# Performance work log

Measured on AMD Instinct MI355X. Metric: run time of the kernel, lower is better.

Reference implementation:

```python
import jax, jax.numpy as jnp
import numpy as np

N_NODES = 100000
N_EDGES = 1600000
IN_FEATS = 128
NUM_HEADS = 4
OUT_FEATS = 32
NUM_ETYPES = 8
DROP_BLOCKS = 4


def setup_inputs() -> dict:
    key = jax.random.key(0)
    k1, k2, k3, k4, k5 = jax.random.split(key, 5)
    feat = jax.random.normal(k1, (N_NODES, IN_FEATS), dtype=jnp.float32)
    e_feat = jax.random.randint(k2, (N_EDGES,), 0, NUM_ETYPES, dtype=jnp.int32)
    src = jax.random.randint(k3, (N_EDGES,), 0, N_NODES, dtype=jnp.int32)
    dst = jax.random.randint(k4, (N_EDGES,), 0, N_NODES, dtype=jnp.int32)
    kf, ke = jax.random.split(k5)
    # xavier_normal with relu gain for fc: std = gain * sqrt(2/(fan_in+fan_out))
    gain = float(np.sqrt(2.0))
    std = gain * float(np.sqrt(2.0 / (IN_FEATS + NUM_HEADS * OUT_FEATS)))
    fc_weight = jax.random.normal(kf, (NUM_HEADS * OUT_FEATS, IN_FEATS), dtype=jnp.float32) * std
    # edge_emb initialized with normal_()
    edge_emb = jax.random.normal(ke, (NUM_ETYPES, NUM_HEADS), dtype=jnp.float32)
    return {"feat": feat, "fc_weight": fc_weight, "edge_emb": edge_emb,
            "e_feat": e_feat, "src": src, "dst": dst, "drop_blocks": DROP_BLOCKS}


def _edge_softmax(e, dst, n_nodes):
    # segmented softmax over incoming edges per destination node, per head
    # e: (E, H)
    m = jax.ops.segment_max(e, dst, num_segments=n_nodes)      # (N, H)
    z = jnp.exp(e - m[dst])                                    # (E, H)
    s = jax.ops.segment_sum(z, dst, num_segments=n_nodes)      # (N, H)
    return z / s[dst]


def reference(feat, fc_weight, edge_emb, e_feat, src, dst, drop_blocks):
    n = feat.shape[0]
    H = edge_emb.shape[1]
    D = fc_weight.shape[0] // H
    # fc projection -> (N, H, D); feat_drop is identity (p=0 / eval)
    ft = (feat @ fc_weight.T).reshape(n, H, D)
    # edge type embedding logits (E, H)
    ee = edge_emb[e_feat]
    attn = _edge_softmax(ee, dst, n)                           # (E, H)
    # mcdropedge with attn_drop p=0: attn broadcast over blocks is identity scaling
    # u_mul_e + sum: gather src features, scale by attn, scatter-sum into dst
    msg = ft[src] * attn[:, :, None]                           # (E, H, D)
    rst = jax.ops.segment_sum(msg, dst, num_segments=n)        # (N, H, D)
    # attn returned with mcdropedge expansion shape (E, H, drop_blocks, 1)
    attn_out = jnp.broadcast_to(attn[:, :, None], (attn.shape[0], H, drop_blocks))[..., None]
    return rst, attn_out
```

## Files before the change

kernel.cpp:

```cpp
#include <hip/hip_runtime.h>


typedef short short8 __attribute__((ext_vector_type(8)));
typedef unsigned short ushort8 __attribute__((ext_vector_type(8)));
typedef float f32x4 __attribute__((ext_vector_type(4)));

__device__ inline unsigned short f2bf(float x) {
    unsigned u = __builtin_bit_cast(unsigned, x);
    u += 0x7FFFu + ((u >> 16) & 1u);
    return (unsigned short)(u >> 16);
}

__device__ inline short8 cvt8(float4 lo, float4 hi) {
    short8 t;
    t[0] = (short)f2bf(lo.x); t[1] = (short)f2bf(lo.y);
    t[2] = (short)f2bf(lo.z); t[3] = (short)f2bf(lo.w);
    t[4] = (short)f2bf(hi.x); t[5] = (short)f2bf(hi.y);
    t[6] = (short)f2bf(hi.z); t[7] = (short)f2bf(hi.w);
    return t;
}

__device__ inline void nt_store4(float* p, float a, float b, float c, float d) {
    f32x4 v = (f32x4){a, b, c, d};
    __builtin_nontemporal_store(v, (f32x4*)p);
}

__global__ __launch_bounds__(256) void k_bcnt(const int* __restrict__ dst,
                                              unsigned* __restrict__ gpart, int E,
                                              const float* __restrict__ W,
                                              unsigned short* __restrict__ Wb) {
    __shared__ unsigned l[256];
    int tid = threadIdx.x;
    if (blockIdx.x < 8) {
        int i = blockIdx.x * 2048 + tid * 8;
        float4 lo = *(const float4*)(W + i);
        float4 hi = *(const float4*)(W + i + 4);
        *(ushort8*)(Wb + i) = __builtin_bit_cast(ushort8, cvt8(lo, hi));
    }
    l[tid] = 0;
    __syncthreads();
    int base = blockIdx.x * 4096;
#pragma unroll
    for (int j = 0; j < 16; ++j) {
        int e = base + j * 256 + tid;
        if (e < E) atomicAdd(&l[(unsigned)dst[e] >> 9], 1u);
    }
    __syncthreads();
    gpart[blockIdx.x * 256 + tid] = l[tid];
}

__global__ __launch_bounds__(256) void k_bscan(const unsigned* __restrict__ gpart,
                                               int nchunk,
                                               unsigned* __restrict__ gbase,
                                               unsigned* __restrict__ gcur) {
    __shared__ unsigned s[256];
    int t = threadIdx.x;
    unsigned sum = 0;
    int r = 0;
    for (; r + 4 <= nchunk; r += 4) {
        unsigned a0 = gpart[(r + 0) * 256 + t];
        unsigned a1 = gpart[(r + 1) * 256 + t];
        unsigned a2 = gpart[(r + 2) * 256 + t];
        unsigned a3 = gpart[(r + 3) * 256 + t];
        sum += a0 + a1 + a2 + a3;
    }
    for (; r < nchunk; ++r) sum += gpart[r * 256 + t];
    unsigned orig = sum;
    s[t] = sum;
    __syncthreads();
    for (int of = 1; of < 256; of <<= 1) {
        unsigned v = (t >= of) ? s[t - of] : 0u;
        __syncthreads();
        s[t] += v;
        __syncthreads();
    }
    unsigned eb = s[t] - orig;
    gbase[t] = eb;
    gcur[t] = eb;
}

__global__ __launch_bounds__(256) void k_partgemm(
        const int* __restrict__ src, const int* __restrict__ dst,
        const int* __restrict__ ef, unsigned* __restrict__ gcur,
        unsigned* __restrict__ csr2, int E, int nbuk, int partBlocks,
        const float* __restrict__ feat, const unsigned short* __restrict__ Wb,
        unsigned short* __restrict__ ftb, int N) {
    __shared__ unsigned short Sb[128 * 136];
    int tid = threadIdx.x;

    if (blockIdx.x < (unsigned)partBlocks) {
        unsigned* lcnt = (unsigned*)Sb;
        unsigned* lbase = lcnt + 256;
        unsigned* lcur = lbase + 256;
        unsigned* gw2 = lcur + 256;
        unsigned* stp = gw2 + 256;
        unsigned short* stb = (unsigned short*)(stp + 4096);
        int bid = blockIdx.x;
        lcnt[tid] = 0;
        __syncthreads();

        int cb = bid * 4096;
        int cc = E - cb; if (cc > 4096) cc = 4096;

        unsigned pay[16];
        unsigned short bk[16];
#pragma unroll
        for (int j = 0; j < 16; ++j) {
            int idx = j * 256 + tid;
            if (idx < cc) {
                int e = cb + idx;
                unsigned d = (unsigned)dst[e];
                pay[j] = (unsigned)src[e] | ((unsigned)ef[e] << 17) | ((d & 511u) << 20);
                bk[j] = (unsigned short)(d >> 9);
                atomicAdd(&lcnt[bk[j]], 1u);
            }
        }
        __syncthreads();
        lbase[tid] = lcnt[tid];
        __syncthreads();
        for (int of = 1; of < 256; of <<= 1) {
            unsigned v = (tid >= of) ? lbase[tid - of] : 0u;
            __syncthreads();
            lbase[tid] += v;
            __syncthreads();
        }
        unsigned eb = lbase[tid] - lcnt[tid];
        __syncthreads();
        lbase[tid] = eb;
        lcur[tid] = eb;
        __syncthreads();
#pragma unroll
        for (int j = 0; j < 16; ++j) {
            int idx = j * 256 + tid;
            if (idx < cc) {
                unsigned lpos = atomicAdd(&lcur[bk[j]], 1u);
                stp[lpos] = pay[j];
                stb[lpos] = bk[j];
            }
        }
        if (tid < nbuk && lcnt[tid]) gw2[tid] = atomicAdd(&gcur[tid], lcnt[tid]);
        __syncthreads();
#pragma unroll
        for (int j = 0; j < 16; ++j) {
            int i = j * 256 + tid;
            if (i < cc) {
                unsigned b = stb[i];
                csr2[gw2[b] + (i - lbase[b])] = stp[i];
            }
        }
        return;
    }

    int row0 = (blockIdx.x - partBlocks) * 128;

#pragma unroll
    for (int it = 0; it < 8; ++it) {
        int idx = it * 2048 + tid * 8;
        int r = idx >> 7, c = idx & 127;
        ushort8 v = *(const ushort8*)(Wb + idx);
        *(ushort8*)((char*)Sb + (((unsigned)(r * 256 + c * 2)) ^ (unsigned)((r & 7) << 4))) = v;
    }
    __syncthreads();

    int wv = tid >> 6, lane = tid & 63;
    int rl = lane & 15;
    unsigned swz = (unsigned)((lane & 7) << 4);
    int kq = (lane >> 4) * 16;
    int ko = (lane >> 4) * 8;

    int ra0 = row0 + wv * 32 + rl;
    int ra1 = ra0 + 16;
    int rc0 = ra0 < N - 1 ? ra0 : N - 1;
    int rc1 = ra1 < N - 1 ? ra1 : N - 1;
    const float* ap0 = feat + (size_t)rc0 * 128 + ko;
    const float* ap1 = feat + (size_t)rc1 * 128 + ko;

    f32x4 acc[2][8];
#pragma unroll
    for (int rt = 0; rt < 2; ++rt)
#pragma unroll
        for (int jt = 0; jt < 8; ++jt)
            acc[rt][jt] = (f32x4){0.f, 0.f, 0.f, 0.f};

    const char* Bb = (const char*)Sb;

    float4 l0 = *(const float4*)(ap0);
    float4 h0 = *(const float4*)(ap0 + 4);
    float4 l1 = *(const float4*)(ap1);
    float4 h1 = *(const float4*)(ap1 + 4);

#pragma unroll 1
    for (int kk = 0; kk < 4; ++kk) {
        short8 a0 = cvt8(l0, h0);
        short8 a1 = cvt8(l1, h1);
        int kn = kk < 3 ? kk + 1 : 3;
        l0 = *(const float4*)(ap0 + kn * 32);
        h0 = *(const float4*)(ap0 + kn * 32 + 4);
        l1 = *(const float4*)(ap1 + kn * 32);
        h1 = *(const float4*)(ap1 + kn * 32 + 4);
        int kb = kk * 64 + kq;
#pragma unroll
        for (int jt = 0; jt < 8; ++jt) {
            short8 bj = *(const short8*)(Bb + (((unsigned)((jt * 16 + rl) * 256 + kb)) ^ swz));
            acc[0][jt] = __builtin_amdgcn_mfma_f32_16x16x32_bf16(a0, bj, acc[0][jt], 0, 0, 0);
            acc[1][jt] = __builtin_amdgcn_mfma_f32_16x16x32_bf16(a1, bj, acc[1][jt], 0, 0, 0);
        }
    }

    __syncthreads();
#pragma unroll
    for (int rt = 0; rt < 2; ++rt) {
        int rbase = wv * 32 + rt * 16 + ((lane >> 4) << 2);
#pragma unroll
        for (int jt = 0; jt < 8; ++jt) {
            int col = jt * 16 + rl;
#pragma unroll
            for (int rg = 0; rg < 4; ++rg)
                Sb[(rbase + rg) * 136 + col] = f2bf(acc[rt][jt][rg]);
        }
    }
    __syncthreads();
#pragma unroll
    for (int g = 0; g < 8; ++g) {
        int rloc = g * 16 + (tid >> 4);
        int cc = (tid & 15) * 8;
        int gr = row0 + rloc;
        if (gr < N) {
            ushort8 v = *(const ushort8*)(&Sb[rloc * 136 + cc]);
            *(ushort8*)(ftb + (size_t)gr * 128 + cc) = v;
        }
    }
}

__global__ __launch_bounds__(256) void k_bsort2(const unsigned* __restrict__ csr2,
                                                const unsigned* __restrict__ gbase,
                                                const unsigned* __restrict__ gend,
                                                const float* __restrict__ emb,
                                                unsigned* __restrict__ csr,
                                                unsigned* __restrict__ offs,
                                                unsigned* __restrict__ deg,
                                                float* __restrict__ stats, int N) {
    __shared__ unsigned cnt8[512 * 8];
    __shared__ unsigned degL[512];
    __shared__ unsigned offsL[512];
    __shared__ unsigned curL[512];
    __shared__ unsigned tmp[256];
    __shared__ float se[32];
    int b = blockIdx.x, tid = threadIdx.x;
    if (tid < 32) se[tid] = emb[tid];
#pragma unroll
    for (int i = 0; i < 16; ++i) cnt8[i * 256 + tid] = 0u;
    __syncthreads();
    unsigned r0 = gbase[b], r1 = gend[b];
    for (unsigned i = r0 + tid; i < r1; i += 256) {
        unsigned en = csr2[i];
        atomicAdd(&cnt8[((en >> 20) & 511u) * 8u + ((en >> 17) & 7u)], 1u);
    }
    __syncthreads();
    int n0 = tid * 2, n1 = tid * 2 + 1;
    unsigned d0 = 0, d1 = 0;
#pragma unroll
    for (int k = 0; k < 8; ++k) { d0 += cnt8[n0 * 8 + k]; d1 += cnt8[n1 * 8 + k]; }
    degL[n0] = d0; degL[n1] = d1;
    tmp[tid] = d0 + d1;
    __syncthreads();
    for (int of = 1; of < 256; of <<= 1) {
        unsigned v = (tid >= of) ? tmp[tid - of] : 0u;
        __syncthreads();
        tmp[tid] += v;
        __syncthreads();
    }
    unsigned eb = tmp[tid] - (d0 + d1);
    offsL[n0] = eb;        curL[n0] = eb;
    offsL[n1] = eb + d0;   curL[n1] = eb + d0;
#pragma unroll
    for (int q = 0; q < 2; ++q) {
        int nl = tid * 2 + q;
        int gn = b * 512 + nl;
        if (gn < N) {
            offs[gn] = r0 + offsL[nl];
            unsigned dg = degL[nl];
            deg[gn] = dg;
            const unsigned* c = &cnt8[nl * 8];
#pragma unroll
            for (int h = 0; h < 4; ++h) {
                float m = -3.4e38f;
#pragma unroll
                for (int tt = 0; tt < 8; ++tt)
                    if (c[tt]) m = fmaxf(m, se[tt * 4 + h]);
                float s = 0.f;
#pragma unroll
                for (int tt = 0; tt < 8; ++tt)
                    if (c[tt]) s += (float)c[tt] * expf(se[tt * 4 + h] - m);
                stats[(size_t)gn * 8 + h] = m;
                stats[(size_t)gn * 8 + 4 + h] = dg ? (1.0f / s) : 0.0f;
            }
        }
    }
    __syncthreads();
    for (unsigned i = r0 + tid; i < r1; i += 256) {
        unsigned en = csr2[i];
        unsigned nlo = (en >> 20) & 511u;
        unsigned tt = (en >> 17) & 7u;
        unsigned pos = r0 + atomicAdd(&curL[nlo], 1u);
        csr[pos] = (en & 0x1FFFFu) | (tt << 20);
    }
}

__global__ __launch_bounds__(256) void k_aggattn(
        const unsigned* __restrict__ csr, const unsigned* __restrict__ offs,
        const unsigned* __restrict__ deg, const float* __restrict__ stats,
        const float* __restrict__ emb, const uint4* __restrict__ ft4,
        float* __restrict__ rst, int N, int aggBlocks,
        const int* __restrict__ e_feat, const int* __restrict__ dst,
        float* __restrict__ ao, int E) {
    __shared__ float sbuf[4 * 257];
    int tid = threadIdx.x;

    if (blockIdx.x >= (unsigned)aggBlocks) {
        int bid = blockIdx.x - aggBlocks;
        int e = bid * 256 + tid;
        float a0 = 0.f, a1 = 0.f, a2 = 0.f, a3 = 0.f;
        if (e < E) {
            int tt = e_feat[e];
            int d = dst[e];
            const float4* st4 = (const float4*)(stats + (size_t)d * 8);
            float4 m4 = st4[0], i4 = st4[1];
            float4 ee = *(const float4*)(emb + tt * 4);
            a0 = expf(ee.x - m4.x) * i4.x;
            a1 = expf(ee.y - m4.y) * i4.y;
            a2 = expf(ee.z - m4.z) * i4.z;
            a3 = expf(ee.w - m4.w) * i4.w;
        }
        sbuf[0 * 257 + tid] = a0;
        sbuf[1 * 257 + tid] = a1;
        sbuf[2 * 257 + tid] = a2;
        sbuf[3 * 257 + tid] = a3;
        __syncthreads();
        size_t base = (size_t)bid * 1024;
        size_t lim = (size_t)E * 4;
#pragma unroll
        for (int r = 0; r < 4; ++r) {
            size_t g = base + r * 256 + tid;
            if (g < lim) {
                int gl = r * 256 + tid;
                float v = sbuf[(gl & 3) * 257 + (gl >> 2)];
                nt_store4(ao + g * 4, v, v, v, v);
            }
        }
        return;
    }

    float* wl = sbuf;
    int wv = tid >> 6, lane = tid & 63;
    int n = blockIdx.x * 4 + wv;
    n = __builtin_amdgcn_readfirstlane(n);
    if (n < N && lane < 32) {
        int tt = lane >> 2, hh = lane & 3;
        float m = stats[(size_t)n * 8 + hh];
        float is = stats[(size_t)n * 8 + 4 + hh];
        wl[wv * 32 + lane] = expf(emb[tt * 4 + hh] - m) * is;
    }
    __syncthreads();
    if (n >= N) return;
    unsigned o = offs[n], dg = deg[n];
    int cl = lane & 15;
    int es = lane >> 4;
    int h = cl >> 2;
    const float* wlh = wl + wv * 32 + h;
    float acc[8];
#pragma unroll
    for (int i = 0; i < 8; ++i) acc[i] = 0.f;

    for (unsigned kb = 0; kb < dg; kb += 64) {
        unsigned rem = dg - kb; if (rem > 64) rem = 64;
        unsigned centry = 0;
        if (lane < (int)rem) centry = csr[o + kb + lane];
        unsigned g = 0;
        for (; g + 16 <= rem; g += 16) {
            uint4 f[4]; float a[4];
#pragma unroll
            for (int q = 0; q < 4; ++q) {
                unsigned e = __shfl(centry, (int)(g + q * 4 + es), 64);
                f[q] = ft4[(size_t)(e & 0xFFFFFu) * 16 + cl];
                a[q] = wlh[(e >> 20) * 4];
            }
#pragma unroll
            for (int q = 0; q < 4; ++q) {
                acc[0] = fmaf(a[q], __builtin_bit_cast(float, f[q].x << 16), acc[0]);
                acc[1] = fmaf(a[q], __builtin_bit_cast(float, f[q].x & 0xFFFF0000u), acc[1]);
                acc[2] = fmaf(a[q], __builtin_bit_cast(float, f[q].y << 16), acc[2]);
                acc[3] = fmaf(a[q], __builtin_bit_cast(float, f[q].y & 0xFFFF0000u), acc[3]);
                acc[4] = fmaf(a[q], __builtin_bit_cast(float, f[q].z << 16), acc[4]);
                acc[5] = fmaf(a[q], __builtin_bit_cast(float, f[q].z & 0xFFFF0000u), acc[5]);
                acc[6] = fmaf(a[q], __builtin_bit_cast(float, f[q].w << 16), acc[6]);
                acc[7] = fmaf(a[q], __builtin_bit_cast(float, f[q].w & 0xFFFF0000u), acc[7]);
            }
        }
        for (; g < rem; g += 4) {
            int eidx = (int)g + es;
            bool valid = eidx < (int)rem;
            unsigned e = __shfl(centry, valid ? eidx : (int)g, 64);
            uint4 f = ft4[(size_t)(e & 0xFFFFFu) * 16 + cl];
            float a = valid ? wlh[(e >> 20) * 4] : 0.f;
            acc[0] = fmaf(a, __builtin_bit_cast(float, f.x << 16), acc[0]);
            acc[1] = fmaf(a, __builtin_bit_cast(float, f.x & 0xFFFF0000u), acc[1]);
            acc[2] = fmaf(a, __builtin_bit_cast(float, f.y << 16), acc[2]);
            acc[3] = fmaf(a, __builtin_bit_cast(float, f.y & 0xFFFF0000u), acc[3]);
            acc[4] = fmaf(a, __builtin_bit_cast(float, f.z << 16), acc[4]);
            acc[5] = fmaf(a, __builtin_bit_cast(float, f.z & 0xFFFF0000u), acc[5]);
            acc[6] = fmaf(a, __builtin_bit_cast(float, f.w << 16), acc[6]);
            acc[7] = fmaf(a, __builtin_bit_cast(float, f.w & 0xFFFF0000u), acc[7]);
        }
    }
#pragma unroll
    for (int i = 0; i < 8; ++i) {
        acc[i] += __shfl_xor(acc[i], 16, 64);
        acc[i] += __shfl_xor(acc[i], 32, 64);
    }
    if (lane < 16) {
        float* op = rst + (size_t)n * 128 + cl * 8;
        nt_store4(op, acc[0], acc[1], acc[2], acc[3]);
        nt_store4(op + 4, acc[4], acc[5], acc[6], acc[7]);
    }
}

extern "C" void kernel_launch(void* const* d_in, const int* in_sizes, int n_in,
                              void* d_out, int out_size, void* d_ws, size_t ws_size,
                              hipStream_t stream) {
    const float* feat = (const float*)d_in[0];
    const float* W = (const float*)d_in[1];
    const float* emb = (const float*)d_in[2];
    const int* e_feat = (const int*)d_in[3];
    const int* src = (const int*)d_in[4];
    const int* dst = (const int*)d_in[5];
    int N = in_sizes[0] / 128;
    int E = in_sizes[3];
    int nbuk = (N + 511) >> 9;
    int nchunk = (E + 4095) / 4096;
    int gemmBlocks = (N + 127) / 128;
    int aggBlocks = (N + 3) / 4;
    int attnBlocks = (E + 255) / 256;

    char* ws = (char*)d_ws;
    size_t off = 0;
    auto alloc = [&](size_t bytes) {
        void* p = ws + off;
        off = (off + bytes + 255) & ~(size_t)255;
        return p;
    };
    unsigned short* ftb = (unsigned short*)alloc((size_t)N * 128 * 2);
    unsigned short* Wb = (unsigned short*)alloc((size_t)in_sizes[1] * 2);
    float* stats = (float*)alloc((size_t)N * 8 * 4);
    unsigned* deg = (unsigned*)alloc((size_t)N * 4);
    unsigned* offs = (unsigned*)alloc((size_t)N * 4);
    unsigned* csr = (unsigned*)alloc((size_t)E * 4);
    unsigned* csr2 = (unsigned*)alloc((size_t)E * 4);
    unsigned* gpart = (unsigned*)alloc((size_t)nchunk * 256 * 4);
    unsigned* gbase = (unsigned*)alloc(256 * 4);
    unsigned* gcur = (unsigned*)alloc(256 * 4);

    float* rst = (float*)d_out;
    float* ao = (float*)d_out + (size_t)N * 128;

    k_bcnt<<<nchunk, 256, 0, stream>>>(dst, gpart, E, W, Wb);
    k_bscan<<<1, 256, 0, stream>>>(gpart, nchunk, gbase, gcur);
    k_partgemm<<<nchunk + gemmBlocks, 256, 0, stream>>>(
        src, dst, e_feat, gcur, csr2, E, nbuk, nchunk, feat, Wb, ftb, N);
    k_bsort2<<<nbuk, 256, 0, stream>>>(csr2, gbase, gcur, emb, csr, offs, deg, stats, N);
    k_aggattn<<<aggBlocks + attnBlocks, 256, 0, stream>>>(
        csr, offs, deg, stats, emb, (const uint4*)ftb, rst, N, aggBlocks,
        e_feat, dst, ao, E);
}
```

Before: 164.6 us.

## Rebalance work granularity across fused partition/GEMM and aggregation/attention kernels

The fused partition+GEMM kernel now puts GEMM blocks first and halves each GEMM tile to 64 rows. All A-operand loads are issued before the weight-staging barrier, so global loads overlap the shared-memory fill. In the aggregation kernel each wave handles two destination nodes in turn, and each attention-output block processes four 256-edge chunks, cutting block count and per-block setup. The aim is better load balance, more GEMM parallelism and less launch/prologue overhead. The cost is more serial work per block and possible tail imbalance in the aggregation.

```diff
diff --git a/kernel.cpp b/kernel.cpp
--- a/kernel.cpp
+++ b/kernel.cpp
@@ -82,24 +82,25 @@
 __global__ __launch_bounds__(256) void k_partgemm(
         const int* __restrict__ src, const int* __restrict__ dst,
         const int* __restrict__ ef, unsigned* __restrict__ gcur,
-        unsigned* __restrict__ csr2, int E, int nbuk, int partBlocks,
+        unsigned* __restrict__ csr2, int E, int nbuk, int gemmBlocks,
         const float* __restrict__ feat, const unsigned short* __restrict__ Wb,
         unsigned short* __restrict__ ftb, int N) {
     __shared__ unsigned short Sb[128 * 136];
     int tid = threadIdx.x;
-
-    if (blockIdx.x < (unsigned)partBlocks) {
+    int bid = blockIdx.x;
+
+    if (bid >= gemmBlocks) {
         unsigned* lcnt = (unsigned*)Sb;
         unsigned* lbase = lcnt + 256;
         unsigned* lcur = lbase + 256;
         unsigned* gw2 = lcur + 256;
         unsigned* stp = gw2 + 256;
         unsigned short* stb = (unsigned short*)(stp + 4096);
-        int bid = blockIdx.x;
+        int rid = bid - gemmBlocks;
         lcnt[tid] = 0;
         __syncthreads();
 
-        int cb = bid * 4096;
+        int cb = rid * 4096;
         int cc = E - cb; if (cc > 4096) cc = 4096;
 
         unsigned pay[16];
@@ -151,7 +152,7 @@
         return;
     }
 
-    int row0 = (blockIdx.x - partBlocks) * 128;
+    int row0 = bid * 64;
 
 #pragma unroll
     for (int it = 0; it < 8; ++it) {
@@ -160,7 +161,6 @@
         ushort8 v = *(const ushort8*)(Wb + idx);
         *(ushort8*)((char*)Sb + (((unsigned)(r * 256 + c * 2)) ^ (unsigned)((r & 7) << 4))) = v;
     }
-    __syncthreads();
 
     int wv = tid >> 6, lane = tid & 63;
     int rl = lane & 15;
@@ -168,60 +168,46 @@
     int kq = (lane >> 4) * 16;
     int ko = (lane >> 4) * 8;
 
-    int ra0 = row0 + wv * 32 + rl;
-    int ra1 = ra0 + 16;
-    int rc0 = ra0 < N - 1 ? ra0 : N - 1;
-    int rc1 = ra1 < N - 1 ? ra1 : N - 1;
-    const float* ap0 = feat + (size_t)rc0 * 128 + ko;
-    const float* ap1 = feat + (size_t)rc1 * 128 + ko;
-
-    f32x4 acc[2][8];
-#pragma unroll
-    for (int rt = 0; rt < 2; ++rt)
-#pragma unroll
-        for (int jt = 0; jt < 8; ++jt)
-            acc[rt][jt] = (f32x4){0.f, 0.f, 0.f, 0.f};
+    int ra = row0 + wv * 16 + rl;
+    int rc = ra < N - 1 ? ra : N - 1;
+    const float* ap = feat + (size_t)rc * 128 + ko;
+
+    float4 f[8];
+#pragma unroll
+    for (int kk = 0; kk < 4; ++kk) {
+        f[2 * kk]     = *(const float4*)(ap + kk * 32);
+        f[2 * kk + 1] = *(const float4*)(ap + kk * 32 + 4);
+    }
+    __syncthreads();
+
+    f32x4 acc[8];
+#pragma unroll
+    for (int jt = 0; jt < 8; ++jt) acc[jt] = (f32x4){0.f, 0.f, 0.f, 0.f};
 
     const char* Bb = (const char*)Sb;
-
-    float4 l0 = *(const float4*)(ap0);
-    float4 h0 = *(const float4*)(ap0 + 4);
-    float4 l1 = *(const float4*)(ap1);
-    float4 h1 = *(const float4*)(ap1 + 4);
-
-#pragma unroll 1
+#pragma unroll
     for (int kk = 0; kk < 4; ++kk) {
-        short8 a0 = cvt8(l0, h0);
-        short8 a1 = cvt8(l1, h1);
-        int kn = kk < 3 ? kk + 1 : 3;
-        l0 = *(const float4*)(ap0 + kn * 32);
-        h0 = *(const float4*)(ap0 + kn * 32 + 4);
-        l1 = *(const float4*)(ap1 + kn * 32);
-        h1 = *(const float4*)(ap1 + kn * 32 + 4);
+        short8 a = cvt8(f[2 * kk], f[2 * kk + 1]);
         int kb = kk * 64 + kq;
 #pragma unroll
         for (int jt = 0; jt < 8; ++jt) {
             short8 bj = *(const short8*)(Bb + (((unsigned)((jt * 16 + rl) * 256 + kb)) ^ swz));
-            acc[0][jt] = __builtin_amdgcn_mfma_f32_16x16x32_bf16(a0, bj, acc[0][jt], 0, 0, 0);
-            acc[1][jt] = __builtin_amdgcn_mfma_f32_16x16x32_bf16(a1, bj, acc[1][jt], 0, 0, 0);
-        }
-    }
-
-    __syncthreads();
-#pragma unroll
-    for (int rt = 0; rt < 2; ++rt) {
-        int rbase = wv * 32 + rt * 16 + ((lane >> 4) << 2);
-#pragma unroll
-        for (int jt = 0; jt < 8; ++jt) {
-            int col = jt * 16 + rl;
-#pragma unroll
-            for (int rg = 0; rg < 4; ++rg)
-                Sb[(rbase + rg) * 136 + col] = f2bf(acc[rt][jt][rg]);
-        }
-    }
-    __syncthreads();
-#pragma unroll
-    for (int g = 0; g < 8; ++g) {
+            acc[jt] = __builtin_amdgcn_mfma_f32_16x16x32_bf16(a, bj, acc[jt], 0, 0, 0);
+        }
+    }
+
+    __syncthreads();
+#pragma unroll
+    for (int jt = 0; jt < 8; ++jt) {
+        int col = jt * 16 + rl;
+        int rbase = wv * 16 + ((lane >> 4) << 2);
+#pragma unroll
+        for (int rg = 0; rg < 4; ++rg)
+            Sb[(rbase + rg) * 136 + col] = f2bf(acc[jt][rg]);
+    }
+    __syncthreads();
+#pragma unroll
+    for (int g = 0; g < 4; ++g) {
         int rloc = g * 16 + (tid >> 4);
         int cc = (tid & 15) * 8;
         int gr = row0 + rloc;
@@ -316,36 +302,41 @@
         float* __restrict__ ao, int E) {
     __shared__ float sbuf[4 * 257];
     int tid = threadIdx.x;
-
-    if (blockIdx.x >= (unsigned)aggBlocks) {
-        int bid = blockIdx.x - aggBlocks;
-        int e = bid * 256 + tid;
-        float a0 = 0.f, a1 = 0.f, a2 = 0.f, a3 = 0.f;
-        if (e < E) {
-            int tt = e_feat[e];
-            int d = dst[e];
-            const float4* st4 = (const float4*)(stats + (size_t)d * 8);
-            float4 m4 = st4[0], i4 = st4[1];
-            float4 ee = *(const float4*)(emb + tt * 4);
-            a0 = expf(ee.x - m4.x) * i4.x;
-            a1 = expf(ee.y - m4.y) * i4.y;
-            a2 = expf(ee.z - m4.z) * i4.z;
-            a3 = expf(ee.w - m4.w) * i4.w;
-        }
-        sbuf[0 * 257 + tid] = a0;
-        sbuf[1 * 257 + tid] = a1;
-        sbuf[2 * 257 + tid] = a2;
-        sbuf[3 * 257 + tid] = a3;
-        __syncthreads();
-        size_t base = (size_t)bid * 1024;
+    int bid = blockIdx.x;
+
+    if (bid >= aggBlocks) {
+        int rid = bid - aggBlocks;
         size_t lim = (size_t)E * 4;
-#pragma unroll
-        for (int r = 0; r < 4; ++r) {
-            size_t g = base + r * 256 + tid;
-            if (g < lim) {
-                int gl = r * 256 + tid;
-                float v = sbuf[(gl & 3) * 257 + (gl >> 2)];
-                nt_store4(ao + g * 4, v, v, v, v);
+#pragma unroll 1
+        for (int r4 = 0; r4 < 4; ++r4) {
+            int e = (rid * 4 + r4) * 256 + tid;
+            float a0 = 0.f, a1 = 0.f, a2 = 0.f, a3 = 0.f;
+            if (e < E) {
+                int tt = e_feat[e];
+                int d = dst[e];
+                const float4* st4 = (const float4*)(stats + (size_t)d * 8);
+                float4 m4 = st4[0], i4 = st4[1];
+                float4 ee = *(const float4*)(emb + tt * 4);
+                a0 = expf(ee.x - m4.x) * i4.x;
+                a1 = expf(ee.y - m4.y) * i4.y;
+                a2 = expf(ee.z - m4.z) * i4.z;
+                a3 = expf(ee.w - m4.w) * i4.w;
+            }
+            __syncthreads();
+            sbuf[0 * 257 + tid] = a0;
+            sbuf[1 * 257 + tid] = a1;
+            sbuf[2 * 257 + tid] = a2;
+            sbuf[3 * 257 + tid] = a3;
+            __syncthreads();
+            size_t base = (size_t)(rid * 4 + r4) * 1024;
+#pragma unroll
+            for (int r = 0; r < 4; ++r) {
+                size_t g = base + r * 256 + tid;
+                if (g < lim) {
+                    int gl = r * 256 + tid;
+                    float v = sbuf[(gl & 3) * 257 + (gl >> 2)];
+                    nt_store4(ao + g * 4, v, v, v, v);
+                }
             }
         }
         return;
@@ -353,75 +344,84 @@
 
     float* wl = sbuf;
     int wv = tid >> 6, lane = tid & 63;
-    int n = blockIdx.x * 4 + wv;
-    n = __builtin_amdgcn_readfirstlane(n);
-    if (n < N && lane < 32) {
-        int tt = lane >> 2, hh = lane & 3;
-        float m = stats[(size_t)n * 8 + hh];
-        float is = stats[(size_t)n * 8 + 4 + hh];
-        wl[wv * 32 + lane] = expf(emb[tt * 4 + hh] - m) * is;
-    }
-    __syncthreads();
-    if (n >= N) return;
-    unsigned o = offs[n], dg = deg[n];
+    int nbase = (bid * 4 + wv) * 2;
+    {
+        int nn = lane >> 5;
+        int idx = lane & 31;
+        int n = nbase + nn;
+        if (n < N) {
+            int tt = idx >> 2, hh = idx & 3;
+            float m = stats[(size_t)n * 8 + hh];
+            float is = stats[(size_t)n * 8 + 4 + hh];
+            wl[wv * 64 + lane] = expf(emb[tt * 4 + hh] - m) * is;
+        }
+    }
+    __syncthreads();
     int cl = lane & 15;
     int es = lane >> 4;
     int h = cl >> 2;
-    const float* wlh = wl + wv * 32 + h;
-    float acc[8];
-#pragma unroll
-    for (int i = 0; i < 8; ++i) acc[i] = 0.f;
-
-    for (unsigned kb = 0; kb < dg; kb += 64) {
-        unsigned rem = dg - kb; if (rem > 64) rem = 64;
-        unsigned centry = 0;
-        if (lane < (int)rem) centry = csr[o + kb + lane];
-        unsigned g = 0;
-        for (; g + 16 <= rem; g += 16) {
-            uint4 f[4]; float a[4];
-#pragma unroll
-            for (int q = 0; q < 4; ++q) {
-                unsigned e = __shfl(centry, (int)(g + q * 4 + es), 64);
-                f[q] = ft4[(size_t)(e & 0xFFFFFu) * 16 + cl];
-                a[q] = wlh[(e >> 20) * 4];
-            }
-#pragma unroll
-            for (int q = 0; q < 4; ++q) {
-                acc[0] = fmaf(a[q], __builtin_bit_cast(float, f[q].x << 16), acc[0]);
-                acc[1] = fmaf(a[q], __builtin_bit_cast(float, f[q].x & 0xFFFF0000u), acc[1]);
-                acc[2] = fmaf(a[q], __builtin_bit_cast(float, f[q].y << 16), acc[2]);
-                acc[3] = fmaf(a[q], __builtin_bit_cast(float, f[q].y & 0xFFFF0000u), acc[3]);
-                acc[4] = fmaf(a[q], __builtin_bit_cast(float, f[q].z << 16), acc[4]);
-                acc[5] = fmaf(a[q], __builtin_bit_cast(float, f[q].z & 0xFFFF0000u), acc[5]);
-                acc[6] = fmaf(a[q], __builtin_bit_cast(float, f[q].w << 16), acc[6]);
-                acc[7] = fmaf(a[q], __builtin_bit_cast(float, f[q].w & 0xFFFF0000u), acc[7]);
-            }
-        }
-        for (; g < rem; g += 4) {
-            int eidx = (int)g + es;
-            bool valid = eidx < (int)rem;
-            unsigned e = __shfl(centry, valid ? eidx : (int)g, 64);
-            uint4 f = ft4[(size_t)(e & 0xFFFFFu) * 16 + cl];
-            float a = valid ? wlh[(e >> 20) * 4] : 0.f;
-            acc[0] = fmaf(a, __builtin_bit_cast(float, f.x << 16), acc[0]);
-            acc[1] = fmaf(a, __builtin_bit_cast(float, f.x & 0xFFFF0000u), acc[1]);
-            acc[2] = fmaf(a, __builtin_bit_cast(float, f.y << 16), acc[2]);
-            acc[3] = fmaf(a, __builtin_bit_cast(float, f.y & 0xFFFF0000u), acc[3]);
-            acc[4] = fmaf(a, __builtin_bit_cast(float, f.z << 16), acc[4]);
-            acc[5] = fmaf(a, __builtin_bit_cast(float, f.z & 0xFFFF0000u), acc[5]);
-            acc[6] = fmaf(a, __builtin_bit_cast(float, f.w << 16), acc[6]);
-            acc[7] = fmaf(a, __builtin_bit_cast(float, f.w & 0xFFFF0000u), acc[7]);
-        }
-    }
-#pragma unroll
-    for (int i = 0; i < 8; ++i) {
-        acc[i] += __shfl_xor(acc[i], 16, 64);
-        acc[i] += __shfl_xor(acc[i], 32, 64);
-    }
-    if (lane < 16) {
-        float* op = rst + (size_t)n * 128 + cl * 8;
-        nt_store4(op, acc[0], acc[1], acc[2], acc[3]);
-        nt_store4(op + 4, acc[4], acc[5], acc[6], acc[7]);
+
+#pragma unroll 1
+    for (int nn = 0; nn < 2; ++nn) {
+        int n = __builtin_amdgcn_readfirstlane(nbase + nn);
+        if (n >= N) break;
+        unsigned o = offs[n], dg = deg[n];
+        const float* wlh = wl + wv * 64 + nn * 32 + h;
+        float acc[8];
+#pragma unroll
+        for (int i = 0; i < 8; ++i) acc[i] = 0.f;
+
+        for (unsigned kb = 0; kb < dg; kb += 64) {
+            unsigned rem = dg - kb; if (rem > 64) rem = 64;
+            unsigned centry = 0;
+            if (lane < (int)rem) centry = csr[o + kb + lane];
+            unsigned g = 0;
+            for (; g + 16 <= rem; g += 16) {
+                uint4 f[4]; float a[4];
+#pragma unroll
+                for (int q = 0; q < 4; ++q) {
+                    unsigned e = __shfl(centry, (int)(g + q * 4 + es), 64);
+                    f[q] = ft4[(size_t)(e & 0xFFFFFu) * 16 + cl];
+                    a[q] = wlh[(e >> 20) * 4];
+                }
+#pragma unroll
+                for (int q = 0; q < 4; ++q) {
+                    acc[0] = fmaf(a[q], __builtin_bit_cast(float, f[q].x << 16), acc[0]);
+                    acc[1] = fmaf(a[q], __builtin_bit_cast(float, f[q].x & 0xFFFF0000u), acc[1]);
+                    acc[2] = fmaf(a[q], __builtin_bit_cast(float, f[q].y << 16), acc[2]);
+                    acc[3] = fmaf(a[q], __builtin_bit_cast(float, f[q].y & 0xFFFF0000u), acc[3]);
+                    acc[4] = fmaf(a[q], __builtin_bit_cast(float, f[q].z << 16), acc[4]);
+                    acc[5] = fmaf(a[q], __builtin_bit_cast(float, f[q].z & 0xFFFF0000u), acc[5]);
+                    acc[6] = fmaf(a[q], __builtin_bit_cast(float, f[q].w << 16), acc[6]);
+                    acc[7] = fmaf(a[q], __builtin_bit_cast(float, f[q].w & 0xFFFF0000u), acc[7]);
+                }
+            }
+            for (; g < rem; g += 4) {
+                int eidx = (int)g + es;
+                bool valid = eidx < (int)rem;
+                unsigned e = __shfl(centry, valid ? eidx : (int)g, 64);
+                uint4 f = ft4[(size_t)(e & 0xFFFFFu) * 16 + cl];
+                float a = valid ? wlh[(e >> 20) * 4] : 0.f;
+                acc[0] = fmaf(a, __builtin_bit_cast(float, f.x << 16), acc[0]);
+                acc[1] = fmaf(a, __builtin_bit_cast(float, f.x & 0xFFFF0000u), acc[1]);
+                acc[2] = fmaf(a, __builtin_bit_cast(float, f.y << 16), acc[2]);
+                acc[3] = fmaf(a, __builtin_bit_cast(float, f.y & 0xFFFF0000u), acc[3]);
+                acc[4] = fmaf(a, __builtin_bit_cast(float, f.z << 16), acc[4]);
+                acc[5] = fmaf(a, __builtin_bit_cast(float, f.z & 0xFFFF0000u), acc[5]);
+                acc[6] = fmaf(a, __builtin_bit_cast(float, f.w << 16), acc[6]);
+                acc[7] = fmaf(a, __builtin_bit_cast(float, f.w & 0xFFFF0000u), acc[7]);
+            }
+        }
+#pragma unroll
+        for (int i = 0; i < 8; ++i) {
+            acc[i] += __shfl_xor(acc[i], 16, 64);
+            acc[i] += __shfl_xor(acc[i], 32, 64);
+        }
+        if (lane < 16) {
+            float* op = rst + (size_t)n * 128 + cl * 8;
+            nt_store4(op, acc[0], acc[1], acc[2], acc[3]);
+            nt_store4(op + 4, acc[4], acc[5], acc[6], acc[7]);
+        }
     }
 }
 
@@ -438,9 +438,9 @@
     int E = in_sizes[3];
     int nbuk = (N + 511) >> 9;
     int nchunk = (E + 4095) / 4096;
-    int gemmBlocks = (N + 127) / 128;
-    int aggBlocks = (N + 3) / 4;
-    int attnBlocks = (E + 255) / 256;
+    int gemmBlocks = (N + 63) / 64;
+    int aggBlocks = (N + 7) / 8;
+    int attnBlocks = (E + 1023) / 1024;
 
     char* ws = (char*)d_ws;
     size_t off = 0;
@@ -465,8 +465,8 @@
 
     k_bcnt<<<nchunk, 256, 0, stream>>>(dst, gpart, E, W, Wb);
     k_bscan<<<1, 256, 0, stream>>>(gpart, nchunk, gbase, gcur);
-    k_partgemm<<<nchunk + gemmBlocks, 256, 0, stream>>>(
-        src, dst, e_feat, gcur, csr2, E, nbuk, nchunk, feat, Wb, ftb, N);
+    k_partgemm<<<gemmBlocks + nchunk, 256, 0, stream>>>(
+        src, dst, e_feat, gcur, csr2, E, nbuk, gemmBlocks, feat, Wb, ftb, N);
     k_bsort2<<<nbuk, 256, 0, stream>>>(csr2, gbase, gcur, emb, csr, offs, deg, stats, N);
     k_aggattn<<<aggBlocks + attnBlocks, 256, 0, stream>>>(
         csr, offs, deg, stats, emb, (const uint4*)ftb, rst, N, aggBlocks,
```

Measured after the change: 167.1 us. About the same (+1.5%).
